# Kernel tuning notes

Measured on AMD Instinct MI355X. Metric: run time of the kernel, lower is better.

Reference implementation:

```python
import jax, jax.numpy as jnp
import numpy as np

B, T, D, H = 4, 2048, 1024, 16
DK = D // H
LN_EPS = 1e-5


def setup_inputs() -> dict:
    key = jax.random.key(0)
    ks = jax.random.split(key, 12)
    s = 1.0 / np.sqrt(D)
    inp = {
        'x': jax.random.normal(ks[0], (B, T, D), jnp.float32),
        'Wq': jax.random.normal(ks[1], (D, D), jnp.float32) * s,
        'bq': jnp.zeros((D,), jnp.float32),
        'Wk': jax.random.normal(ks[2], (D, D), jnp.float32) * s,
        'bk': jnp.zeros((D,), jnp.float32),
        'Wv': jax.random.normal(ks[3], (D, D), jnp.float32) * s,
        'bv': jnp.zeros((D,), jnp.float32),
        'Wo': jax.random.normal(ks[4], (D, D), jnp.float32) * s,
        'bo': jnp.zeros((D,), jnp.float32),
        'ln_g': jnp.ones((D,), jnp.float32),
        'ln_b': jnp.zeros((D,), jnp.float32),
    }
    return inp


def reference(x, Wq, bq, Wk, bk, Wv, bv, Wo, bo, ln_g, ln_b):
    b, t, d = x.shape
    scale = jnp.sqrt(jnp.asarray(DK, x.dtype))
    # QKV projections -> [b, h, t, dk]
    q = (x @ Wq + bq).reshape(b, t, H, DK).transpose(0, 2, 1, 3)
    k = (x @ Wk + bk).reshape(b, t, H, DK).transpose(0, 2, 1, 3)
    v = (x @ Wv + bv).reshape(b, t, H, DK).transpose(0, 2, 1, 3)
    scores = jnp.einsum('bhqd,bhkd->bhqk', q, k) / scale  # [b,h,t,t]
    mask = jnp.tril(jnp.ones((t, t), x.dtype))[None, None]  # [1,1,t,t]
    neg = jnp.finfo(x.dtype).min
    scores = jnp.where(mask == 0, neg, scores)
    attn = jax.nn.softmax(scores, axis=-1)
    # mask-renormalize (as in the torch module)
    attn = attn * mask
    denom = attn.sum(-1, keepdims=True)
    attn = jnp.where(denom > 0, attn / denom, jnp.zeros_like(attn))
    ctx = jnp.einsum('bhqk,bhkd->bhqd', attn, v)  # [b,h,t,dk]
    ctx = ctx.transpose(0, 2, 1, 3).reshape(b, t, d)
    out = ctx @ Wo + bo
    y = out + x  # residual
    mu = y.mean(-1, keepdims=True)
    var = ((y - mu) ** 2).mean(-1, keepdims=True)
    return (y - mu) / jnp.sqrt(var + LN_EPS) * ln_g + ln_b
```

## Files before the change

kernel.cpp:

```cpp
#include <hip/hip_runtime.h>


using u16 = unsigned short;
using u32 = unsigned int;
typedef _Float16 f16x8 __attribute__((ext_vector_type(8)));
typedef __fp16 h16x2 __attribute__((ext_vector_type(2)));
typedef float f32x4 __attribute__((ext_vector_type(4)));
typedef unsigned short u16x8 __attribute__((ext_vector_type(8)));
typedef unsigned short u16x4 __attribute__((ext_vector_type(4)));
typedef unsigned int u32x4 __attribute__((ext_vector_type(4)));

template <bool B> struct BoolTag { static constexpr bool v = B; };

__device__ inline u16 f2h_bits(float f) {
    _Float16 h = (_Float16)f;
    return __builtin_bit_cast(u16, h);
}
__device__ inline float h2f(u16 u) {
    return (float)__builtin_bit_cast(_Float16, u);
}

__device__ __forceinline__ void gload16(const void* g, void* l) {
    __builtin_amdgcn_global_load_lds(
        (const __attribute__((address_space(1))) void*)g,
        (__attribute__((address_space(3))) void*)l, 16, 0, 0);
}

__global__ __launch_bounds__(256) void convert_kernel(
    const float* __restrict__ x, u16* __restrict__ xb,
    const float* __restrict__ W0, const float* __restrict__ W1,
    const float* __restrict__ W2, const float* __restrict__ W3,
    u16* __restrict__ Wt) {
    __shared__ float ts[64][68];
    const int bid = blockIdx.x, tid = threadIdx.x;
    if (bid < 4096) {
        size_t i = ((size_t)bid * 256 + tid) * 8;
        float4 a = *(const float4*)(x + i);
        float4 b = *(const float4*)(x + i + 4);
        u16x8 o;
        o[0] = f2h_bits(a.x); o[1] = f2h_bits(a.y); o[2] = f2h_bits(a.z); o[3] = f2h_bits(a.w);
        o[4] = f2h_bits(b.x); o[5] = f2h_bits(b.y); o[6] = f2h_bits(b.z); o[7] = f2h_bits(b.w);
        *(u16x8*)(xb + i) = o;
        return;
    }
    const int wb = bid - 4096;
    const int z = wb >> 8, rem = wb & 255;
    const float* W = z == 0 ? W0 : (z == 1 ? W1 : (z == 2 ? W2 : W3));
    u16* Wo = Wt + (size_t)z * 1048576;
    const int k0 = (rem >> 4) * 64, n0 = (rem & 15) * 64;
    const int rr = tid >> 3, c = tid & 7;
#pragma unroll
    for (int p = 0; p < 2; p++) {
        int k = p * 32 + rr;
        float4 u = *(const float4*)(W + (size_t)(k0 + k) * 1024 + n0 + c * 8);
        float4 w = *(const float4*)(W + (size_t)(k0 + k) * 1024 + n0 + c * 8 + 4);
        *(float4*)&ts[k][c * 8] = u;
        *(float4*)&ts[k][c * 8 + 4] = w;
    }
    __syncthreads();
#pragma unroll
    for (int p = 0; p < 2; p++) {
        int n = p * 32 + rr;
        u16 o[8];
#pragma unroll
        for (int j = 0; j < 8; j++) o[j] = f2h_bits(ts[c * 8 + j][n]);
        *(u16x8*)(Wo + (size_t)(n0 + n) * 1024 + k0 + c * 8) = *(u16x8*)o;
    }
}

template <int MODE>
__global__ __launch_bounds__(512) void gemm256_kernel(
    const u16* __restrict__ A, const u16* __restrict__ Wt,
    const float* __restrict__ b0, const float* __restrict__ b1,
    const float* __restrict__ b2, u16* __restrict__ qo, u16* __restrict__ ko,
    u16* __restrict__ vt) {
    constexpr int NBY = (MODE == 0) ? 12 : 4;
    __shared__ u16 As[3][128 * 64];
    __shared__ u16 Bs[3][256 * 64];

    const int bid = blockIdx.x;
    const int cpx = (MODE == 0) ? 96 : 32;
    const int swz = (bid & 7) * cpx + (bid >> 3);
    const int bx = swz / NBY, by = swz % NBY;
    const size_t row0 = (size_t)bx * 128;
    const size_t col0 = (size_t)by * 256;

    const int tid = threadIdx.x, lane = tid & 63;
    const int wid = tid >> 6, wm = wid >> 2, wn = wid & 3;
    const int l15 = lane & 15, lg = lane >> 4;
    const int rr = tid >> 3, c8 = tid & 7;
    const int scw = (c8 ^ (rr & 7)) * 8;

    f32x4 acc[4][4] = {};

    auto stage_half = [&](int kt, u16* dA, u16* dB, int h) {
        const int k0 = kt * 64;
        if (h == 0) {
            gload16(A + (row0 + rr) * 1024 + k0 + scw, dA + tid * 8);
            gload16(Wt + (col0 + rr) * 1024 + k0 + scw, dB + tid * 8);
            gload16(Wt + (col0 + 64 + rr) * 1024 + k0 + scw, dB + (512 + tid) * 8);
        } else {
            gload16(A + (row0 + 64 + rr) * 1024 + k0 + scw, dA + (512 + tid) * 8);
            gload16(Wt + (col0 + 128 + rr) * 1024 + k0 + scw, dB + (1024 + tid) * 8);
            gload16(Wt + (col0 + 192 + rr) * 1024 + k0 + scw, dB + (1536 + tid) * 8);
        }
    };

    auto ldops = [&](const u16* bA, const u16* bB, int kcv, f16x8* Af, f16x8* Bf) {
        const int swo = ((kcv * 4 + lg) ^ (l15 & 7)) * 8;
#pragma unroll
        for (int n = 0; n < 4; n++)
            Bf[n] = *(const f16x8*)(bB + (wn * 64 + n * 16 + l15) * 64 + swo);
#pragma unroll
        for (int m = 0; m < 4; m++)
            Af[m] = *(const f16x8*)(bA + (wm * 64 + m * 16 + l15) * 64 + swo);
    };

    auto domfma = [&](const f16x8* Af, const f16x8* Bf) {
        __builtin_amdgcn_s_setprio(1);
#pragma unroll
        for (int m = 0; m < 4; m++)
#pragma unroll
            for (int n = 0; n < 4; n++)
                acc[m][n] = __builtin_amdgcn_mfma_f32_16x16x32_f16(
                    Af[m], Bf[n], acc[m][n], 0, 0, 0);
        __builtin_amdgcn_s_setprio(0);
    };

    u16 *pA = &As[0][0], *pnA = &As[1][0], *ppA = &As[2][0];
    u16 *pB = &Bs[0][0], *pnB = &Bs[1][0], *ppB = &Bs[2][0];

    stage_half(0, pA, pB, 0);
    stage_half(0, pA, pB, 1);
    stage_half(1, pnA, pnB, 0);
    stage_half(1, pnA, pnB, 1);
    asm volatile("s_waitcnt vmcnt(6)" ::: "memory");
    __builtin_amdgcn_sched_barrier(0);
    __builtin_amdgcn_s_barrier();

#pragma unroll 1
    for (int t = 0; t < 16; t++) {
        f16x8 af[4], bf[4];
        ldops(pA, pB, 0, af, bf);
        if (t < 14) stage_half(t + 2, ppA, ppB, 0);
        __builtin_amdgcn_sched_barrier(0);
        __builtin_amdgcn_s_barrier();
        asm volatile("s_waitcnt lgkmcnt(0)" ::: "memory");
        __builtin_amdgcn_sched_barrier(0);
        domfma(af, bf);
        __builtin_amdgcn_sched_barrier(0);
        __builtin_amdgcn_s_barrier();
        ldops(pA, pB, 1, af, bf);
        if (t < 14) stage_half(t + 2, ppA, ppB, 1);
        if (t < 14)       asm volatile("s_waitcnt vmcnt(6)" ::: "memory");
        else if (t == 14) asm volatile("s_waitcnt vmcnt(0)" ::: "memory");
        __builtin_amdgcn_sched_barrier(0);
        __builtin_amdgcn_s_barrier();
        asm volatile("s_waitcnt lgkmcnt(0)" ::: "memory");
        __builtin_amdgcn_sched_barrier(0);
        domfma(af, bf);
        __builtin_amdgcn_sched_barrier(0);
        if (t < 15) {
            __builtin_amdgcn_s_barrier();
            u16* tp;
            tp = pA; pA = pnA; pnA = ppA; ppA = tp;
            tp = pB; pB = pnB; pnB = ppB; ppB = tp;
        }
    }

    if (MODE == 0) {
        const int zsel = by >> 2;
        if (zsel < 2) {
            u16* ob = zsel == 0 ? qo : ko;
            const float* bias = zsel == 0 ? b0 : b1;
            const float qs = zsel == 0 ? 0.18033688f : 1.0f;
#pragma unroll
            for (int m = 0; m < 4; m++) {
#pragma unroll
                for (int n = 0; n < 4; n++) {
                    size_t col = col0 + wn * 64 + n * 16 + l15;
                    size_t colz = col & 1023;
                    float bb = bias[colz];
#pragma unroll
                    for (int r = 0; r < 4; r++) {
                        size_t row = row0 + wm * 64 + m * 16 + lg * 4 + r;
                        ob[row * 1024 + colz] = f2h_bits((acc[m][n][r] + bb) * qs);
                    }
                }
            }
        } else {
            u16* TL = &Bs[0][0];
            __syncthreads();
#pragma unroll
            for (int m = 0; m < 4; m++) {
#pragma unroll
                for (int n = 0; n < 4; n++) {
                    int cl = wn * 64 + n * 16 + l15;
                    float bb = b2[(col0 & 1023) + cl];
#pragma unroll
                    for (int r = 0; r < 4; r++) {
                        int rl = wm * 64 + m * 16 + lg * 4 + r;
                        TL[cl * 134 + rl] = f2h_bits(acc[m][n][r] + bb);
                    }
                }
            }
            __syncthreads();
            const int vrl = tid >> 1, th = tid & 1;
            size_t vrow = (row0 >> 11) * 1024 + (col0 & 1023) + vrl;
            const int t0loc = (int)(row0 & 2047) + th * 64;
#pragma unroll
            for (int j = 0; j < 8; j++)
                *(u16x8*)(vt + vrow * 2048 + t0loc + j * 8) =
                    *(const u16x8*)(TL + vrl * 134 + th * 64 + j * 8);
        }
    } else {
        u16* yo = qo;
        const u16* xres = ko;
#pragma unroll
        for (int m = 0; m < 4; m++) {
#pragma unroll
            for (int n = 0; n < 4; n++) {
                size_t col = col0 + wn * 64 + n * 16 + l15;
                float bb = b0[col];
#pragma unroll
                for (int r = 0; r < 4; r++) {
                    size_t row = row0 + wm * 64 + m * 16 + lg * 4 + r;
                    size_t idx = row * 1024 + col;
                    yo[idx] = f2h_bits(acc[m][n][r] + bb + h2f(xres[idx]));
                }
            }
        }
    }
}

__global__ __launch_bounds__(512) void attn_kernel(const u16* __restrict__ Q,
                                                   const u16* __restrict__ Kb,
                                                   const u16* __restrict__ Vt,
                                                   u16* __restrict__ ctx) {
    __shared__ u16 Ks[2][128 * 64];
    __shared__ u16 Vs[2][64 * 128];

    const int i = (int)blockIdx.x;
    const int bh = i & 63;
    const int sel = (i >> 6) & 3;
    const int qb = (i < 256) ? (7 - sel) : sel;
    const int b = bh >> 4, h = bh & 15;
    const int tid = threadIdx.x, lane = tid & 63, wid = tid >> 6;
    const int l15 = lane & 15, lg = lane >> 4;
    const int q0w = qb * 256 + wid * 32;
    const int send = qb * 256;

    const int rr = tid >> 3, c8 = tid & 7;
    const int scw = (c8 ^ (rr & 7)) * 8;
    const int vr = tid >> 4, vc = tid & 15;
    const int scv = (vc ^ (vr & 15)) * 8;
    const size_t kbase = ((size_t)b * 2048) * 1024 + h * 64 + scw;
    const size_t vbase0 = ((size_t)bh * 64 + vr) * 2048 + scv;
    const size_t vbase1 = ((size_t)bh * 64 + vr + 32) * 2048 + scv;

    f16x8 qv[2][2];
#pragma unroll
    for (int qf = 0; qf < 2; qf++) {
        size_t qoff = ((size_t)b * 2048 + q0w + qf * 16 + l15) * 1024 + h * 64 + lg * 8;
        qv[qf][0] = *(const f16x8*)(Q + qoff);
        qv[qf][1] = *(const f16x8*)(Q + qoff + 32);
    }

    const int swk0 = (lg ^ (l15 & 7)) * 8;
    const int swk1 = ((4 + lg) ^ (l15 & 7)) * 8;

    const h16x2 one2 = {(__fp16)1.0f, (__fp16)1.0f};

    f32x4 acc[2][4] = {};
    float psum[2] = {0.0f, 0.0f};

    auto stage = [&](int s, int bf) {
        gload16(Kb + kbase + (size_t)(s + rr) * 1024, Ks[bf] + tid * 8);
        gload16(Kb + kbase + (size_t)(s + rr + 64) * 1024, Ks[bf] + (512 + tid) * 8);
        gload16(Vt + vbase0 + s, Vs[bf] + tid * 8);
        gload16(Vt + vbase1 + s, Vs[bf] + (512 + tid) * 8);
    };

    auto body = [&](int s, int bf, auto maskc) {
        constexpr bool MASK = decltype(maskc)::v;
        u32 W[2][8][2];
#pragma unroll
        for (int c = 0; c < 8; c++) {
            const u16* kp = Ks[bf] + (c * 16 + l15) * 64;
            f16x8 kf0 = *(const f16x8*)(kp + swk0);
            f16x8 kf1 = *(const f16x8*)(kp + swk1);
#pragma unroll
            for (int qf = 0; qf < 2; qf++) {
                f32x4 z = {};
                z = __builtin_amdgcn_mfma_f32_16x16x32_f16(kf0, qv[qf][0], z, 0, 0, 0);
                z = __builtin_amdgcn_mfma_f32_16x16x32_f16(kf1, qv[qf][1], z, 0, 0, 0);
                float p0 = __builtin_amdgcn_exp2f(z[0]);
                float p1 = __builtin_amdgcn_exp2f(z[1]);
                float p2 = __builtin_amdgcn_exp2f(z[2]);
                float p3 = __builtin_amdgcn_exp2f(z[3]);
                if (MASK) {
                    int kk = s + c * 16 + lg * 4;
                    int qq = q0w + qf * 16 + l15;
                    p0 = (kk + 0 <= qq) ? p0 : 0.0f;
                    p1 = (kk + 1 <= qq) ? p1 : 0.0f;
                    p2 = (kk + 2 <= qq) ? p2 : 0.0f;
                    p3 = (kk + 3 <= qq) ? p3 : 0.0f;
                }
                h16x2 w0 = __builtin_amdgcn_cvt_pkrtz(p0, p1);
                h16x2 w1 = __builtin_amdgcn_cvt_pkrtz(p2, p3);
                psum[qf] = __builtin_amdgcn_fdot2(w0, one2, psum[qf], false);
                psum[qf] = __builtin_amdgcn_fdot2(w1, one2, psum[qf], false);
                W[qf][c][0] = __builtin_bit_cast(u32, w0);
                W[qf][c][1] = __builtin_bit_cast(u32, w1);
            }
        }
        f16x8 pa0[2][2], pa1[2][2];
#pragma unroll
        for (int qf = 0; qf < 2; qf++) {
#pragma unroll
            for (int hf = 0; hf < 2; hf++) {
                const int c0 = hf * 4;
                auto sA = __builtin_amdgcn_permlane32_swap(W[qf][c0][0], W[qf][c0 + 1][0], false, false);
                auto tA = __builtin_amdgcn_permlane16_swap(sA[0], sA[1], false, false);
                auto sB = __builtin_amdgcn_permlane32_swap(W[qf][c0][1], W[qf][c0 + 1][1], false, false);
                auto tB = __builtin_amdgcn_permlane16_swap(sB[0], sB[1], false, false);
                u32x4 v0 = {tA[0], tB[0], tA[1], tB[1]};
                pa0[qf][hf] = __builtin_bit_cast(f16x8, v0);
                auto sC = __builtin_amdgcn_permlane32_swap(W[qf][c0 + 2][0], W[qf][c0 + 3][0], false, false);
                auto tC = __builtin_amdgcn_permlane16_swap(sC[0], sC[1], false, false);
                auto sD = __builtin_amdgcn_permlane32_swap(W[qf][c0 + 2][1], W[qf][c0 + 3][1], false, false);
                auto tD = __builtin_amdgcn_permlane16_swap(sD[0], sD[1], false, false);
                u32x4 v1 = {tC[0], tD[0], tC[1], tD[1]};
                pa1[qf][hf] = __builtin_bit_cast(f16x8, v1);
            }
        }
        __builtin_amdgcn_s_setprio(1);
#pragma unroll
        for (int dt = 0; dt < 4; dt++) {
            const u16* vp = Vs[bf] + (dt * 16 + l15) * 128;
#pragma unroll
            for (int hf = 0; hf < 2; hf++) {
                f16x8 vf0 = *(const f16x8*)(vp + ((hf * 8 + lg) ^ l15) * 8);
                f16x8 vf1 = *(const f16x8*)(vp + ((hf * 8 + 4 + lg) ^ l15) * 8);
#pragma unroll
                for (int qf = 0; qf < 2; qf++) {
                    acc[qf][dt] = __builtin_amdgcn_mfma_f32_16x16x32_f16(
                        pa0[qf][hf], vf0, acc[qf][dt], 0, 0, 0);
                    acc[qf][dt] = __builtin_amdgcn_mfma_f32_16x16x32_f16(
                        pa1[qf][hf], vf1, acc[qf][dt], 0, 0, 0);
                }
            }
        }
        __builtin_amdgcn_s_setprio(0);
    };

    stage(0, 0);
    stage(128, 1);
    asm volatile("s_waitcnt vmcnt(4)" ::: "memory");
    __builtin_amdgcn_sched_barrier(0);
    __builtin_amdgcn_s_barrier();

    int cur = 0;
#pragma unroll 1
    for (int s = 0; s < send; s += 128) {
        body(s, cur, BoolTag<false>{});
        __builtin_amdgcn_sched_barrier(0);
        __builtin_amdgcn_s_barrier();
        stage(s + 256, cur);
        asm volatile("s_waitcnt vmcnt(4)" ::: "memory");
        __builtin_amdgcn_sched_barrier(0);
        __builtin_amdgcn_s_barrier();
        cur ^= 1;
    }
    body(send, cur, BoolTag<true>{});
    __builtin_amdgcn_sched_barrier(0);
    __builtin_amdgcn_s_barrier();
    asm volatile("s_waitcnt vmcnt(0)" ::: "memory");
    __builtin_amdgcn_sched_barrier(0);
    __builtin_amdgcn_s_barrier();
    if (wid >= 4) body(send + 128, cur ^ 1, BoolTag<true>{});

#pragma unroll
    for (int qf = 0; qf < 2; qf++) {
        psum[qf] += __shfl_xor(psum[qf], 16);
        psum[qf] += __shfl_xor(psum[qf], 32);
    }
#pragma unroll
    for (int qf = 0; qf < 2; qf++) {
        float inv = 1.0f / psum[qf];
#pragma unroll
        for (int r = 0; r < 4; r++) {
            float ir = __shfl(inv, lg * 4 + r);
            size_t row = (size_t)b * 2048 + q0w + qf * 16 + lg * 4 + r;
#pragma unroll
            for (int dt = 0; dt < 4; dt++)
                ctx[row * 1024 + h * 64 + dt * 16 + l15] = f2h_bits(acc[qf][dt][r] * ir);
        }
    }
}

__global__ __launch_bounds__(256) void ln_kernel(const u16* __restrict__ y,
                                                 const float* __restrict__ g,
                                                 const float* __restrict__ bb,
                                                 float* __restrict__ out) {
    const int r = blockIdx.x, tid = threadIdx.x;
    u16x4 v4 = *(const u16x4*)(y + (size_t)r * 1024 + tid * 4);
    float vx = h2f(v4[0]), vy = h2f(v4[1]), vz = h2f(v4[2]), vw = h2f(v4[3]);
    float s = vx + vy + vz + vw;
    float sq = vx * vx + vy * vy + vz * vz + vw * vw;
#pragma unroll
    for (int ofs = 1; ofs < 64; ofs <<= 1) {
        s += __shfl_xor(s, ofs);
        sq += __shfl_xor(sq, ofs);
    }
    __shared__ float as[4], aq[4];
    if ((tid & 63) == 0) { as[tid >> 6] = s; aq[tid >> 6] = sq; }
    __syncthreads();
    s = as[0] + as[1] + as[2] + as[3];
    sq = aq[0] + aq[1] + aq[2] + aq[3];
    float mu = s * (1.0f / 1024.0f);
    float var = sq * (1.0f / 1024.0f) - mu * mu;
    float rstd = rsqrtf(var + 1e-5f);
    float4 gv = *(const float4*)(g + tid * 4);
    float4 bv = *(const float4*)(bb + tid * 4);
    float4 o4;
    o4.x = (vx - mu) * rstd * gv.x + bv.x;
    o4.y = (vy - mu) * rstd * gv.y + bv.y;
    o4.z = (vz - mu) * rstd * gv.z + bv.z;
    o4.w = (vw - mu) * rstd * gv.w + bv.w;
    *(float4*)(out + (size_t)r * 1024 + tid * 4) = o4;
}

extern "C" void kernel_launch(void* const* d_in, const int* in_sizes, int n_in,
                              void* d_out, int out_size, void* d_ws, size_t ws_size,
                              hipStream_t stream) {
    const float* x  = (const float*)d_in[0];
    const float* Wq = (const float*)d_in[1];
    const float* bq = (const float*)d_in[2];
    const float* Wk = (const float*)d_in[3];
    const float* bk = (const float*)d_in[4];
    const float* Wv = (const float*)d_in[5];
    const float* bv = (const float*)d_in[6];
    const float* Wo = (const float*)d_in[7];
    const float* bo = (const float*)d_in[8];
    const float* lg = (const float*)d_in[9];
    const float* lb = (const float*)d_in[10];
    float* out = (float*)d_out;

    char* ws = (char*)d_ws;
    u16* xb = (u16*)(ws + 0);
    u16* wt = (u16*)(ws + 16777216);
    u16* q  = (u16*)(ws + 25165824);
    u16* k  = (u16*)(ws + 41943040);
    u16* vt = (u16*)(ws + 75497472);
    u16* cx = (u16*)(ws + 92274688);
    u16* y16 = (u16*)(ws + 109051904);

    convert_kernel<<<5120, 256, 0, stream>>>(x, xb, Wq, Wk, Wv, Wo, wt);

    gemm256_kernel<0><<<768, 512, 0, stream>>>(xb, wt, bq, bk, bv, q, k, vt);
    attn_kernel<<<512, 512, 0, stream>>>(q, k, vt, cx);
    gemm256_kernel<1><<<256, 512, 0, stream>>>(cx, wt + 3145728, bo, nullptr,
                                               nullptr, y16, xb, nullptr);
    ln_kernel<<<8192, 256, 0, stream>>>(y16, lg, lb, out);
}
```

Measured before the change: 167.7 us.

## Shrink GEMM tiles to 128x128 with 4 waves and double-buffered LDS

Replaces the 128x256 tile, 8-wave, triple-buffered GEMM with a 128x128 tile, 4-wave kernel that double-buffers a single 64 KB LDS array and doubles the grid size. The aim is more blocks for better CU occupancy and tail balance, and less LDS per block so more blocks fit per CU. In exchange each block reuses operands less, and the prefetch depth drops to one tile, with a full vmcnt(0) wait every iteration, so global load latency is less hidden.

Result: no change. 169.0 us (+0.8%).

```diff
diff --git a/kernel.cpp b/kernel.cpp
--- a/kernel.cpp
+++ b/kernel.cpp
@@ -69,44 +69,45 @@
 }
 
 template <int MODE>
-__global__ __launch_bounds__(512) void gemm256_kernel(
+__global__ __launch_bounds__(256) void gemm128_kernel(
     const u16* __restrict__ A, const u16* __restrict__ Wt,
     const float* __restrict__ b0, const float* __restrict__ b1,
     const float* __restrict__ b2, u16* __restrict__ qo, u16* __restrict__ ko,
     u16* __restrict__ vt) {
-    constexpr int NBY = (MODE == 0) ? 12 : 4;
-    __shared__ u16 As[3][128 * 64];
-    __shared__ u16 Bs[3][256 * 64];
+    constexpr int NBY = (MODE == 0) ? 24 : 8;
+    __shared__ u16 SH[32768];
 
     const int bid = blockIdx.x;
-    const int cpx = (MODE == 0) ? 96 : 32;
+    const int cpx = (MODE == 0) ? 192 : 64;
     const int swz = (bid & 7) * cpx + (bid >> 3);
     const int bx = swz / NBY, by = swz % NBY;
     const size_t row0 = (size_t)bx * 128;
-    const size_t col0 = (size_t)by * 256;
+    const size_t col0 = (size_t)by * 128;
 
     const int tid = threadIdx.x, lane = tid & 63;
-    const int wid = tid >> 6, wm = wid >> 2, wn = wid & 3;
+    const int wid = tid >> 6, wm = wid >> 1, wn = wid & 1;
     const int l15 = lane & 15, lg = lane >> 4;
     const int rr = tid >> 3, c8 = tid & 7;
     const int scw = (c8 ^ (rr & 7)) * 8;
 
     f32x4 acc[4][4] = {};
 
-    auto stage_half = [&](int kt, u16* dA, u16* dB, int h) {
+    auto stage_tile = [&](int kt, int p) {
         const int k0 = kt * 64;
-        if (h == 0) {
-            gload16(A + (row0 + rr) * 1024 + k0 + scw, dA + tid * 8);
-            gload16(Wt + (col0 + rr) * 1024 + k0 + scw, dB + tid * 8);
-            gload16(Wt + (col0 + 64 + rr) * 1024 + k0 + scw, dB + (512 + tid) * 8);
-        } else {
-            gload16(A + (row0 + 64 + rr) * 1024 + k0 + scw, dA + (512 + tid) * 8);
-            gload16(Wt + (col0 + 128 + rr) * 1024 + k0 + scw, dB + (1024 + tid) * 8);
-            gload16(Wt + (col0 + 192 + rr) * 1024 + k0 + scw, dB + (1536 + tid) * 8);
+        u16* dA = SH + p * 8192;
+        u16* dB = SH + 16384 + p * 8192;
+#pragma unroll
+        for (int g = 0; g < 4; g++) {
+            gload16(A + (row0 + g * 32 + rr) * 1024 + k0 + scw,
+                    dA + (g * 256 + tid) * 8);
+            gload16(Wt + (col0 + g * 32 + rr) * 1024 + k0 + scw,
+                    dB + (g * 256 + tid) * 8);
         }
     };
 
-    auto ldops = [&](const u16* bA, const u16* bB, int kcv, f16x8* Af, f16x8* Bf) {
+    auto ldops = [&](int p, int kcv, f16x8* Af, f16x8* Bf) {
+        const u16* bA = SH + p * 8192;
+        const u16* bB = SH + 16384 + p * 8192;
         const int swo = ((kcv * 4 + lg) ^ (l15 & 7)) * 8;
 #pragma unroll
         for (int n = 0; n < 4; n++)
@@ -127,22 +128,17 @@
         __builtin_amdgcn_s_setprio(0);
     };
 
-    u16 *pA = &As[0][0], *pnA = &As[1][0], *ppA = &As[2][0];
-    u16 *pB = &Bs[0][0], *pnB = &Bs[1][0], *ppB = &Bs[2][0];
-
-    stage_half(0, pA, pB, 0);
-    stage_half(0, pA, pB, 1);
-    stage_half(1, pnA, pnB, 0);
-    stage_half(1, pnA, pnB, 1);
-    asm volatile("s_waitcnt vmcnt(6)" ::: "memory");
+    stage_tile(0, 0);
+    asm volatile("s_waitcnt vmcnt(0)" ::: "memory");
     __builtin_amdgcn_sched_barrier(0);
     __builtin_amdgcn_s_barrier();
 
 #pragma unroll 1
     for (int t = 0; t < 16; t++) {
+        const int cp = t & 1, np = (t + 1) & 1;
         f16x8 af[4], bf[4];
-        ldops(pA, pB, 0, af, bf);
-        if (t < 14) stage_half(t + 2, ppA, ppB, 0);
+        ldops(cp, 0, af, bf);
+        if (t < 15) stage_tile(t + 1, np);
         __builtin_amdgcn_sched_barrier(0);
         __builtin_amdgcn_s_barrier();
         asm volatile("s_waitcnt lgkmcnt(0)" ::: "memory");
@@ -150,26 +146,19 @@
         domfma(af, bf);
         __builtin_amdgcn_sched_barrier(0);
         __builtin_amdgcn_s_barrier();
-        ldops(pA, pB, 1, af, bf);
-        if (t < 14) stage_half(t + 2, ppA, ppB, 1);
-        if (t < 14)       asm volatile("s_waitcnt vmcnt(6)" ::: "memory");
-        else if (t == 14) asm volatile("s_waitcnt vmcnt(0)" ::: "memory");
+        ldops(cp, 1, af, bf);
+        if (t < 15) asm volatile("s_waitcnt vmcnt(0)" ::: "memory");
         __builtin_amdgcn_sched_barrier(0);
         __builtin_amdgcn_s_barrier();
         asm volatile("s_waitcnt lgkmcnt(0)" ::: "memory");
         __builtin_amdgcn_sched_barrier(0);
         domfma(af, bf);
         __builtin_amdgcn_sched_barrier(0);
-        if (t < 15) {
-            __builtin_amdgcn_s_barrier();
-            u16* tp;
-            tp = pA; pA = pnA; pnA = ppA; ppA = tp;
-            tp = pB; pB = pnB; pnB = ppB; ppB = tp;
-        }
+        if (t < 15) __builtin_amdgcn_s_barrier();
     }
 
     if (MODE == 0) {
-        const int zsel = by >> 2;
+        const int zsel = by >> 3;
         if (zsel < 2) {
             u16* ob = zsel == 0 ? qo : ko;
             const float* bias = zsel == 0 ? b0 : b1;
@@ -189,14 +178,15 @@
                 }
             }
         } else {
-            u16* TL = &Bs[0][0];
+            u16* TL = SH;
+            const int dz0 = (by - 16) * 128;
             __syncthreads();
 #pragma unroll
             for (int m = 0; m < 4; m++) {
 #pragma unroll
                 for (int n = 0; n < 4; n++) {
                     int cl = wn * 64 + n * 16 + l15;
-                    float bb = b2[(col0 & 1023) + cl];
+                    float bb = b2[dz0 + cl];
 #pragma unroll
                     for (int r = 0; r < 4; r++) {
                         int rl = wm * 64 + m * 16 + lg * 4 + r;
@@ -205,13 +195,14 @@
                 }
             }
             __syncthreads();
-            const int vrl = tid >> 1, th = tid & 1;
-            size_t vrow = (row0 >> 11) * 1024 + (col0 & 1023) + vrl;
-            const int t0loc = (int)(row0 & 2047) + th * 64;
+            const int vcl = tid >> 1, th = tid & 1;
+            const int b = (int)(row0 >> 11);
+            const int tloc = (int)(row0 & 2047);
+            size_t vrow = (size_t)b * 1024 + dz0 + vcl;
 #pragma unroll
             for (int j = 0; j < 8; j++)
-                *(u16x8*)(vt + vrow * 2048 + t0loc + j * 8) =
-                    *(const u16x8*)(TL + vrl * 134 + th * 64 + j * 8);
+                *(u16x8*)(vt + vrow * 2048 + tloc + th * 64 + j * 8) =
+                    *(const u16x8*)(TL + vcl * 134 + th * 64 + j * 8);
         }
     } else {
         u16* yo = qo;
@@ -458,9 +449,9 @@
 
     convert_kernel<<<5120, 256, 0, stream>>>(x, xb, Wq, Wk, Wv, Wo, wt);
 
-    gemm256_kernel<0><<<768, 512, 0, stream>>>(xb, wt, bq, bk, bv, q, k, vt);
+    gemm128_kernel<0><<<1536, 256, 0, stream>>>(xb, wt, bq, bk, bv, q, k, vt);
     attn_kernel<<<512, 512, 0, stream>>>(q, k, vt, cx);
-    gemm256_kernel<1><<<256, 512, 0, stream>>>(cx, wt + 3145728, bo, nullptr,
+    gemm128_kernel<1><<<512, 256, 0, stream>>>(cx, wt + 3145728, bo, nullptr,
                                                nullptr, y16, xb, nullptr);
     ln_kernel<<<8192, 256, 0, stream>>>(y16, lg, lb, out);
 }
```
